# Kernel tuning notes

Measured on AMD Instinct MI355X. Metric: run time of the kernel, lower is better.

## Reference

```python
import jax, jax.numpy as jnp
import numpy as np


def setup_inputs() -> dict:
    key = jax.random.key(0)
    ks = jax.random.split(key, 6)
    B, S, H, F, E = 4, 2048, 1024, 4096, 8
    x = jax.random.normal(ks[0], (B, S, H), dtype=jnp.float32)
    Wr = jax.random.normal(ks[1], (H, E), dtype=jnp.float32) * (1.0 / np.sqrt(H))
    br = jnp.zeros((E,), dtype=jnp.float32)
    W1 = jax.random.normal(ks[2], (E, H, F), dtype=jnp.float32) * (1.0 / np.sqrt(H))
    b1 = jnp.zeros((E, F), dtype=jnp.float32)
    W2 = jax.random.normal(ks[3], (E, F, H), dtype=jnp.float32) * (1.0 / np.sqrt(F))
    b2 = jnp.zeros((E, H), dtype=jnp.float32)
    b_buf = jnp.zeros((E,), dtype=jnp.float32)  # load-balancing bias buffer, zero-init
    return {"x": x, "b_buf": b_buf, "Wr": Wr, "br": br,
            "W1": W1, "b1": b1, "W2": W2, "b2": b2, "k": 2}


def reference(x, b_buf, Wr, br, W1, b1, W2, b2, k):
    # Router
    scores = jnp.einsum('bsh,he->bse', x, Wr) + br          # [B,S,E]
    probs = jax.nn.softmax(scores, axis=-1)
    # load_balancing: expert selection uses biased scores (b_buf pre-update)
    _, expert_id = jax.lax.top_k(probs + b_buf, k)          # [B,S,k] int
    # combine weights use unbiased probs
    p, _ = jax.lax.top_k(probs, k)                          # [B,S,k]
    # Dense-dispatch reference: run every expert MLP on all tokens,
    # then select via one-hot mask (same math as gather/scatter dispatch).
    h1 = jnp.einsum('bsh,ehf->ebsf', x, W1) + b1[:, None, None, :]
    h1 = jax.nn.gelu(h1, approximate=False)                 # torch nn.GELU = exact
    out_e = jnp.einsum('ebsf,efh->ebsh', h1, W2) + b2[:, None, None, :]
    E = W1.shape[0]
    onehot = (expert_id[None, :, :, :] == jnp.arange(E)[:, None, None, None]).astype(x.dtype)  # [E,B,S,k]
    out_k = jnp.einsum('ebsk,ebsh->bskh', onehot, out_e)    # scatter-combine per slot
    w = p / jnp.sum(p, axis=-1, keepdims=True)              # normalize top-k probs
    return jnp.einsum('bsk,bskh->bsh', w, out_k)
```

## Files before the change

### kernel.cpp

```cpp
#include <hip/hip_runtime.h>
#include <stdint.h>

#define NTOK 8192
#define H_ 1024
#define F_ 4096
#define E_ 8
#define VCAP 18432
#define VMBLK 72
#define NCOMP 16384

using f32x4  = __attribute__((ext_vector_type(4))) float;
using short8 = __attribute__((ext_vector_type(8))) short;

typedef __attribute__((address_space(1))) const uint32_t gu32;
typedef __attribute__((address_space(3))) uint32_t lu32;

__device__ __forceinline__ void glds16(const void* g, void* l) {
  __builtin_amdgcn_global_load_lds((gu32*)g, (lu32*)l, 16, 0, 0);
}

__device__ __forceinline__ ushort f2bf(float f) {
  union { float f; uint32_t u; } v; v.f = f;
  uint32_t r = (v.u + 0x7FFFu + ((v.u >> 16) & 1u)) >> 16;
  return (ushort)r;
}

__device__ __forceinline__ float gelu_t(float x) {
  float u = 0.7978845608028654f * (x + 0.044715f * x * x * x);
  float e = exp2f(u * 2.885390081777927f);
  float th = 1.0f - 2.0f / (1.0f + e);
  return 0.5f * x * (1.0f + th);
}

__global__ void k_init(int* cnt, int* cur, int* tok, float* wl, int* v2c) {
  int i = blockIdx.x * 256 + threadIdx.x;
  if (i < E_) { cnt[i] = 0; cur[i] = 0; }
  if (i < VCAP) { tok[i] = -1; wl[i] = 0.f; v2c[i] = -1; }
}

__global__ __launch_bounds__(256) void k_transcvt(const float* __restrict__ W,
                                                  ushort* __restrict__ WT,
                                                  int R, int C) {
  __shared__ float t[64][65];
  int e = blockIdx.z;
  int c0 = blockIdx.x * 64, r0 = blockIdx.y * 64;
  const float* Wp = W + (size_t)e * R * C;
  ushort* Tp = WT + (size_t)e * R * C;
  int tx = threadIdx.x & 15, ty = threadIdx.x >> 4;
#pragma unroll
  for (int i = 0; i < 4; i++) {
    int lr = ty + i * 16;
    const float4 v = *(const float4*)&Wp[(size_t)(r0 + lr) * C + c0 + tx * 4];
    t[lr][tx * 4 + 0] = v.x; t[lr][tx * 4 + 1] = v.y;
    t[lr][tx * 4 + 2] = v.z; t[lr][tx * 4 + 3] = v.w;
  }
  __syncthreads();
#pragma unroll
  for (int i = 0; i < 4; i++) {
    int lc = ty + i * 16;
    ushort4 o;
    o.x = f2bf(t[tx * 4 + 0][lc]);
    o.y = f2bf(t[tx * 4 + 1][lc]);
    o.z = f2bf(t[tx * 4 + 2][lc]);
    o.w = f2bf(t[tx * 4 + 3][lc]);
    *(ushort4*)&Tp[(size_t)(c0 + lc) * R + r0 + tx * 4] = o;
  }
}

__global__ __launch_bounds__(256) void k_router(const float* __restrict__ x,
                                                const float* __restrict__ Wr,
                                                const float* __restrict__ br,
                                                const float* __restrict__ bbuf,
                                                int* cnt, int* te, float* tw) {
  int wid = threadIdx.x >> 6, lane = threadIdx.x & 63;
  int t = blockIdx.x * 4 + wid;
  const float* xp = x + (size_t)t * H_;
  double acc[E_];
#pragma unroll
  for (int e = 0; e < E_; e++) acc[e] = 0.0;
  for (int j = lane; j < H_; j += 64) {
    float xv = xp[j];
    const float4 w0 = *(const float4*)&Wr[j * 8];
    const float4 w1 = *(const float4*)&Wr[j * 8 + 4];
    acc[0] += (double)xv * (double)w0.x;
    acc[1] += (double)xv * (double)w0.y;
    acc[2] += (double)xv * (double)w0.z;
    acc[3] += (double)xv * (double)w0.w;
    acc[4] += (double)xv * (double)w1.x;
    acc[5] += (double)xv * (double)w1.y;
    acc[6] += (double)xv * (double)w1.z;
    acc[7] += (double)xv * (double)w1.w;
  }
#pragma unroll
  for (int e = 0; e < E_; e++)
    for (int s = 32; s > 0; s >>= 1) acc[e] += __shfl_xor(acc[e], s);
  if (lane == 0) {
    double s[E_], m = -1e300;
    for (int e = 0; e < E_; e++) { s[e] = acc[e] + (double)br[e]; if (s[e] > m) m = s[e]; }
    double pe[E_], sum = 0.0;
    for (int e = 0; e < E_; e++) { pe[e] = exp(s[e] - m); sum += pe[e]; }
    double pr[E_], bb[E_];
    for (int e = 0; e < E_; e++) { pr[e] = pe[e] / sum; bb[e] = pr[e] + (double)bbuf[e]; }
    int e0 = 0;
    for (int e = 1; e < E_; e++) if (bb[e] > bb[e0]) e0 = e;
    int e1 = (e0 == 0) ? 1 : 0;
    for (int e = 0; e < E_; e++) if (e != e0 && bb[e] > bb[e1]) e1 = e;
    int a0 = 0;
    for (int e = 1; e < E_; e++) if (pr[e] > pr[a0]) a0 = e;
    int a1 = (a0 == 0) ? 1 : 0;
    for (int e = 0; e < E_; e++) if (e != a0 && pr[e] > pr[a1]) a1 = e;
    double iv = 1.0 / (pr[a0] + pr[a1]);
    te[t * 2] = e0; te[t * 2 + 1] = e1;
    tw[t * 2] = (float)(pr[a0] * iv); tw[t * 2 + 1] = (float)(pr[a1] * iv);
    atomicAdd(&cnt[e0], 1); atomicAdd(&cnt[e1], 1);
  }
}

__global__ void k_offsets(const int* cnt, int* off, int* coff) {
  if (threadIdx.x == 0 && blockIdx.x == 0) {
    int o = 0, c = 0;
    for (int e = 0; e < E_; e++) {
      off[e] = o; coff[e] = c;
      o += ((cnt[e] + 255) >> 8) << 8;
      c += cnt[e];
    }
    off[E_] = o; coff[E_] = c;
  }
}

__global__ void k_build(const int* __restrict__ te, const float* __restrict__ tw,
                        const int* __restrict__ off, const int* __restrict__ coff,
                        int* cur, int* tok, float* wl, int* v2c, int* ctok) {
  int t = blockIdx.x * 256 + threadIdx.x;
  if (t >= NTOK) return;
#pragma unroll
  for (int s = 0; s < 2; s++) {
    int e = te[t * 2 + s];
    int slot = atomicAdd(&cur[e], 1);
    int vp = off[e] + slot;
    int cp = coff[e] + slot;
    tok[vp] = t; wl[vp] = tw[t * 2 + s]; v2c[vp] = cp; ctok[cp] = t;
  }
}

__global__ __launch_bounds__(256) void k_gather(const float* __restrict__ x,
                                                const int* __restrict__ ctok,
                                                ushort* __restrict__ Xg) {
  int row = blockIdx.x;
  int t = ctok[row];
  const float4* src = (const float4*)(x + (size_t)t * H_);
  ushort4* dst = (ushort4*)(Xg + (size_t)row * H_);
  int i = threadIdx.x;
  float4 v = src[i];
  ushort4 o; o.x = f2bf(v.x); o.y = f2bf(v.y); o.z = f2bf(v.z); o.w = f2bf(v.w);
  dst[i] = o;
}

__global__ void k_zero(float* out) {
  size_t i = (size_t)blockIdx.x * 256 + threadIdx.x;
  float4 z; z.x = 0.f; z.y = 0.f; z.z = 0.f; z.w = 0.f;
  ((float4*)out)[i] = z;
}

template <int MODE>
__global__ __launch_bounds__(512) void k_gemm(const ushort* __restrict__ A,
                                              const ushort* __restrict__ BT,
                                              const float* __restrict__ bias,
                                              ushort* __restrict__ h1,
                                              float* __restrict__ Out,
                                              const int* __restrict__ off,
                                              const int* __restrict__ v2c,
                                              const int* __restrict__ tok,
                                              const float* __restrict__ wl,
                                              int K, int N, int NTe) {
  extern __shared__ char lds[];
  int nwg = gridDim.x;
  int cpx = nwg >> 3;
  int bid = blockIdx.x;
  int lid = (bid & 7) * cpx + (bid >> 3);
  int gsz = NTe << 2;
  int g = lid / gsz, rm = lid % gsz;
  int ne = rm >> 2, m = (g << 2) + (rm & 3);
  int row0 = m << 8;
  if (row0 >= off[E_]) return;
  int e = 0;
  while (off[e + 1] <= row0) e++;
  int n0, k0, nk;
  if (MODE == 0) { n0 = ne << 8; k0 = 0; nk = K >> 6; }
  else           { n0 = (ne >> 1) << 8; k0 = (ne & 1) * (K >> 1); nk = K >> 7; }
  const ushort* Bp = BT + (size_t)e * (size_t)N * (size_t)K;

  int tid = threadIdx.x, lane = tid & 63, w = tid >> 6;
  int wr = w >> 2, wc = w & 3;

  f32x4 acc[8][4];
#pragma unroll
  for (int mm = 0; mm < 8; mm++)
#pragma unroll
    for (int nn = 0; nn < 4; nn++) acc[mm][nn] = (f32x4){0.f, 0.f, 0.f, 0.f};

  int urow = (w << 3) + (lane >> 3);
  int schunk = (lane & 7) ^ (lane >> 3);
  const char *aS0, *aS1, *aS2, *aS3, *bS0, *bS1, *bS2, *bS3;
  {
    int v0 = v2c[row0 + 0 * 64 + urow];   if (v0 < 0) v0 = 0;
    int v1 = v2c[row0 + 1 * 64 + urow];   if (v1 < 0) v1 = 0;
    int v2 = v2c[row0 + 2 * 64 + urow];   if (v2 < 0) v2 = 0;
    int v3 = v2c[row0 + 3 * 64 + urow];   if (v3 < 0) v3 = 0;
    size_t kb = (size_t)k0 * 2 + (size_t)schunk * 16;
    aS0 = (const char*)(A + (size_t)v0 * K) + kb;
    aS1 = (const char*)(A + (size_t)v1 * K) + kb;
    aS2 = (const char*)(A + (size_t)v2 * K) + kb;
    aS3 = (const char*)(A + (size_t)v3 * K) + kb;
    bS0 = (const char*)(Bp + (size_t)(n0 + 0 * 64 + urow) * K) + kb;
    bS1 = (const char*)(Bp + (size_t)(n0 + 1 * 64 + urow) * K) + kb;
    bS2 = (const char*)(Bp + (size_t)(n0 + 2 * 64 + urow) * K) + kb;
    bS3 = (const char*)(Bp + (size_t)(n0 + 3 * 64 + urow) * K) + kb;
  }

  int fr = lane & 15, fq = lane >> 4;
  int frs = fr & 7;

  short8 af_[4][2], bf_[4][2];

#define STG_A(u, tt, bbuf) glds16(aS##u + (size_t)(tt) * 128, lds + (bbuf) * 65536 + (u) * 8192 + (w << 10))
#define STG_B(u, tt, bbuf) glds16(bS##u + (size_t)(tt) * 128, lds + (bbuf) * 65536 + 32768 + (u) * 8192 + (w << 10))

#define RDA(mmq, bbuf) do {                                                  \
    const ushort* LA_ = (const ushort*)(lds + (bbuf) * 65536);               \
    _Pragma("unroll")                                                        \
    for (int i = 0; i < 4; ++i)                                              \
      _Pragma("unroll")                                                      \
      for (int ks = 0; ks < 2; ++ks)                                         \
        af_[i][ks] = *(const short8*)&LA_[((wr << 7) + ((mmq) + i) * 16 + fr) * 64 + (((ks << 2) + fq) ^ frs) * 8]; \
  } while (0)

#define RDB(bbuf) do {                                                       \
    const ushort* LB_ = (const ushort*)(lds + (bbuf) * 65536 + 32768);       \
    _Pragma("unroll")                                                        \
    for (int i = 0; i < 4; ++i)                                              \
      _Pragma("unroll")                                                      \
      for (int ks = 0; ks < 2; ++ks)                                         \
        bf_[i][ks] = *(const short8*)&LB_[((wc << 6) + i * 16 + fr) * 64 + (((ks << 2) + fq) ^ frs) * 8]; \
  } while (0)

#define MMQ(mmq, nnq) do {                                                   \
    __builtin_amdgcn_s_setprio(1);                                           \
    _Pragma("unroll")                                                        \
    for (int i = 0; i < 4; ++i)                                              \
      _Pragma("unroll")                                                      \
      for (int jn = 0; jn < 2; ++jn)                                         \
        _Pragma("unroll")                                                    \
        for (int ks = 0; ks < 2; ++ks)                                       \
          acc[(mmq) + i][(nnq) + jn] = __builtin_amdgcn_mfma_f32_16x16x32_bf16(af_[i][ks], bf_[(nnq) + jn][ks], acc[(mmq) + i][(nnq) + jn], 0, 0, 0); \
    __builtin_amdgcn_s_setprio(0);                                           \
  } while (0)

#define FENCE() __builtin_amdgcn_sched_barrier(0)
#define BAR()   __builtin_amdgcn_s_barrier()
#define WAIT_LGKM() asm volatile("s_waitcnt lgkmcnt(0)" ::: "memory")

  STG_B(0, 0, 0); STG_B(1, 0, 0); STG_B(2, 0, 0); STG_B(3, 0, 0);
  STG_A(0, 0, 0); STG_A(1, 0, 0); STG_A(2, 0, 0); STG_A(3, 0, 0);
  if (nk > 1) {
    STG_B(0, 1, 1); STG_B(1, 1, 1); STG_B(2, 1, 1); STG_B(3, 1, 1);
    STG_A(0, 1, 1); STG_A(2, 1, 1);
  }

  for (int T = 0; T < nk; ++T) {
    int bb = T & 1, nb = bb ^ 1;
    bool s1 = (T + 1 < nk), s2 = (T + 2 < nk);
    if (s1) { STG_A(1, T + 1, nb); STG_A(3, T + 1, nb); }
    if (s1) asm volatile("s_waitcnt vmcnt(8)" ::: "memory");
    else    asm volatile("s_waitcnt vmcnt(0)" ::: "memory");
    BAR(); FENCE();
    RDA(0, bb); RDB(bb);
    WAIT_LGKM(); FENCE();
    BAR(); FENCE();
    MMQ(0, 0);
    if (s2) { STG_B(0, T + 2, bb); STG_B(1, T + 2, bb); }
    MMQ(0, 2);
    if (s2) { STG_B(2, T + 2, bb); STG_B(3, T + 2, bb); }
    RDA(4, bb);
    WAIT_LGKM(); FENCE();
    BAR(); FENCE();
    MMQ(4, 0);
    if (s2) { STG_A(0, T + 2, bb); STG_A(2, T + 2, bb); }
    MMQ(4, 2);
  }
#undef STG_A
#undef STG_B
#undef RDA
#undef RDB
#undef MMQ
#undef FENCE
#undef BAR
#undef WAIT_LGKM

  const float* bp = bias + (size_t)e * N;
  int cb = n0 + (wc << 6);
  if (MODE == 0) {
#pragma unroll
    for (int mm = 0; mm < 8; mm++) {
#pragma unroll
      for (int j = 0; j < 4; j++) {
        int vr = row0 + (wr << 7) + mm * 16 + (fq << 2) + j;
        int cr = v2c[vr];
        if (cr < 0) continue;
        ushort* hp = h1 + (size_t)cr * N + cb;
#pragma unroll
        for (int nn = 0; nn < 4; nn++) {
          float v = acc[mm][nn][j] + bp[cb + nn * 16 + fr];
          hp[nn * 16 + fr] = f2bf(gelu_t(v));
        }
      }
    }
  } else {
    bool addb = (k0 == 0);
#pragma unroll
    for (int mm = 0; mm < 8; mm++) {
#pragma unroll
      for (int j = 0; j < 4; j++) {
        int vr = row0 + (wr << 7) + mm * 16 + (fq << 2) + j;
        int t2 = tok[vr];
        if (t2 < 0) continue;
        float wgt = wl[vr];
#pragma unroll
        for (int nn = 0; nn < 4; nn++) {
          int c = cb + nn * 16 + fr;
          float v = acc[mm][nn][j] + (addb ? bp[c] : 0.f);
          atomicAdd(&Out[(size_t)t2 * (size_t)N + c], wgt * v);
        }
      }
    }
  }
}

extern "C" void kernel_launch(void* const* d_in, const int* in_sizes, int n_in,
                              void* d_out, int out_size, void* d_ws, size_t ws_size,
                              hipStream_t stream) {
  (void)in_sizes; (void)n_in; (void)out_size; (void)ws_size;
  const float* x    = (const float*)d_in[0];
  const float* bbuf = (const float*)d_in[1];
  const float* Wr   = (const float*)d_in[2];
  const float* br   = (const float*)d_in[3];
  const float* W1   = (const float*)d_in[4];
  const float* b1   = (const float*)d_in[5];
  const float* W2   = (const float*)d_in[6];
  const float* b2   = (const float*)d_in[7];
  float* out = (float*)d_out;

  char* ws = (char*)d_ws;
  ushort* W1T = (ushort*)ws;
  ushort* W2T = (ushort*)(ws + 67108864);
  ushort* Xg  = (ushort*)(ws + 134217728);
  ushort* h1  = (ushort*)(ws + 167772160);
  char* meta  = ws + 301989888;
  int*   cnt  = (int*)(meta);
  int*   off  = (int*)(meta + 64);
  int*   coff = (int*)(meta + 128);
  int*   cur  = (int*)(meta + 192);
  int*   te   = (int*)(meta + 256);
  float* tw   = (float*)(meta + 65792);
  int*   tok  = (int*)(meta + 131328);
  float* wl   = (float*)(meta + 205056);
  int*   v2c  = (int*)(meta + 278784);
  int*   ctok = (int*)(meta + 352512);

  hipFuncSetAttribute((const void*)&k_gemm<0>,
                      hipFuncAttributeMaxDynamicSharedMemorySize, 131072);
  hipFuncSetAttribute((const void*)&k_gemm<1>,
                      hipFuncAttributeMaxDynamicSharedMemorySize, 131072);

  k_init<<<VMBLK, 256, 0, stream>>>(cnt, cur, tok, wl, v2c);
  k_transcvt<<<dim3(F_ / 64, H_ / 64, E_), 256, 0, stream>>>(W1, W1T, H_, F_);
  k_transcvt<<<dim3(H_ / 64, F_ / 64, E_), 256, 0, stream>>>(W2, W2T, F_, H_);
  k_router<<<NTOK / 4, 256, 0, stream>>>(x, Wr, br, bbuf, cnt, te, tw);
  k_offsets<<<1, 64, 0, stream>>>(cnt, off, coff);
  k_build<<<NTOK / 256, 256, 0, stream>>>(te, tw, off, coff, cur, tok, wl, v2c, ctok);
  k_gather<<<NCOMP, 256, 0, stream>>>(x, ctok, Xg);
  k_zero<<<(NTOK * H_ / 4) / 256, 256, 0, stream>>>(out);
  k_gemm<0><<<16 * VMBLK, 512, 131072, stream>>>(Xg, W1T, b1, h1, nullptr,
                                                 off, v2c, nullptr, nullptr,
                                                 H_, F_, 16);
  k_gemm<1><<<8 * VMBLK, 512, 131072, stream>>>(h1, W2T, b2, nullptr, out,
                                                off, v2c, tok, wl,
                                                F_, H_, 8);
}
```

Baseline: 998.5 us.

## Simplify GEMM main loop to single-stage prefetch with one barrier per tile

Replaces the two-stage-ahead staggered prefetch schedule with a simpler double buffer. The whole next tile is issued at the start of each iteration, and the loop waits on vmcnt(0) plus one barrier at the end. The explicit lgkmcnt waits and the mid-iteration barriers around the LDS fragment reads are removed, cutting synchronisation overhead. In exchange there is less load lookahead, and global-to-LDS writes into the next buffer are no longer interleaved with the MFMA phases.

```diff
diff --git a/kernel.cpp b/kernel.cpp
--- a/kernel.cpp
+++ b/kernel.cpp
@@ -258,35 +258,29 @@
 
 #define FENCE() __builtin_amdgcn_sched_barrier(0)
 #define BAR()   __builtin_amdgcn_s_barrier()
-#define WAIT_LGKM() asm volatile("s_waitcnt lgkmcnt(0)" ::: "memory")
 
   STG_B(0, 0, 0); STG_B(1, 0, 0); STG_B(2, 0, 0); STG_B(3, 0, 0);
   STG_A(0, 0, 0); STG_A(1, 0, 0); STG_A(2, 0, 0); STG_A(3, 0, 0);
-  if (nk > 1) {
-    STG_B(0, 1, 1); STG_B(1, 1, 1); STG_B(2, 1, 1); STG_B(3, 1, 1);
-    STG_A(0, 1, 1); STG_A(2, 1, 1);
-  }
+  asm volatile("s_waitcnt vmcnt(0)" ::: "memory");
+  BAR(); FENCE();
 
   for (int T = 0; T < nk; ++T) {
     int bb = T & 1, nb = bb ^ 1;
-    bool s1 = (T + 1 < nk), s2 = (T + 2 < nk);
-    if (s1) { STG_A(1, T + 1, nb); STG_A(3, T + 1, nb); }
-    if (s1) asm volatile("s_waitcnt vmcnt(8)" ::: "memory");
-    else    asm volatile("s_waitcnt vmcnt(0)" ::: "memory");
-    BAR(); FENCE();
+    bool pre = (T + 1 < nk);
+    if (pre) {
+      STG_B(0, T + 1, nb); STG_B(1, T + 1, nb);
+      STG_B(2, T + 1, nb); STG_B(3, T + 1, nb);
+      STG_A(0, T + 1, nb); STG_A(1, T + 1, nb);
+      STG_A(2, T + 1, nb); STG_A(3, T + 1, nb);
+    }
     RDA(0, bb); RDB(bb);
-    WAIT_LGKM(); FENCE();
-    BAR(); FENCE();
-    MMQ(0, 0);
-    if (s2) { STG_B(0, T + 2, bb); STG_B(1, T + 2, bb); }
-    MMQ(0, 2);
-    if (s2) { STG_B(2, T + 2, bb); STG_B(3, T + 2, bb); }
+    MMQ(0, 0); MMQ(0, 2);
     RDA(4, bb);
-    WAIT_LGKM(); FENCE();
-    BAR(); FENCE();
-    MMQ(4, 0);
-    if (s2) { STG_A(0, T + 2, bb); STG_A(2, T + 2, bb); }
-    MMQ(4, 2);
+    MMQ(4, 0); MMQ(4, 2);
+    if (pre) {
+      asm volatile("s_waitcnt vmcnt(0)" ::: "memory");
+      BAR(); FENCE();
+    }
   }
 #undef STG_A
 #undef STG_B
@@ -295,7 +289,6 @@
 #undef MMQ
 #undef FENCE
 #undef BAR
-#undef WAIT_LGKM
 
   const float* bp = bias + (size_t)e * N;
   int cb = n0 + (wc << 6);
```

After: 996.6 us. About the same (-0.2%).
